# Optimization experiments

Hardware: AMD Instinct MI355X
Metric: run time of the kernel (lower is better)

Reference implementation:

```python
import jax, jax.numpy as jnp
import numpy as np

OUT_DIM = 512

def setup_inputs() -> dict:
    key = jax.random.key(0)
    ks = jax.random.split(key, 8)
    B, C1, C2, H, W, D = 8, 768, 768, 48, 48, OUT_DIM
    x = jax.random.normal(ks[0], (B, C1, H, W), dtype=jnp.float32)
    xt = jax.random.normal(ks[1], (B, C2, H, W), dtype=jnp.float32)
    # nn.Linear params: weight [out, in], bias [out]
    def lin(k, fan_in, fan_out):
        bound = 1.0 / np.sqrt(fan_in)
        kw, kb = jax.random.split(k)
        w = jax.random.uniform(kw, (fan_out, fan_in), jnp.float32, -bound, bound)
        b = jax.random.uniform(kb, (fan_out,), jnp.float32, -bound, bound)
        return w, b
    wq, bq = lin(ks[2], C1, D)
    wk, bk = lin(ks[3], C2, D)
    wv, bv = lin(ks[4], C2, D)
    return {"x": x, "xt": xt, "wq": wq, "bq": bq, "wk": wk, "bk": bk, "wv": wv, "bv": bv}

def reference(x, xt, wq, bq, wk, bk, wv, bv):
    B, C1, H, W = x.shape
    D = wq.shape[0]
    # flatten(2).transpose(1,2): [B, C, H, W] -> [B, H*W, C]
    xs = x.reshape(B, C1, H * W).transpose(0, 2, 1)
    xts = xt.reshape(B, xt.shape[1], -1).transpose(0, 2, 1)
    Q = jnp.einsum('bsc,dc->bsd', xs, wq) + bq   # [B, S, D]
    K = jnp.einsum('btc,dc->btd', xts, wk) + bk  # [B, T, D]
    V = jnp.einsum('btc,dc->btd', xts, wv) + bv  # [B, T, D]
    scores = jnp.einsum('bsd,btd->bst', Q, K) / jnp.sqrt(jnp.float32(D))
    attn = jax.nn.softmax(scores, axis=-1)  # dropout omitted (eval mode)
    return jnp.einsum('bst,btd->bsd', attn, V)
```

## Files before the change

kernel.cpp:

```cpp
#include <hip/hip_runtime.h>
#include <stdint.h>


typedef __bf16 bf16x8 __attribute__((ext_vector_type(8)));
typedef float f32x4 __attribute__((ext_vector_type(4)));

__device__ __forceinline__ unsigned short f2bf(float f) {
  union { float f; unsigned int u; } c; c.f = f;
  return (unsigned short)((c.u + 0x7fffu + ((c.u >> 16) & 1u)) >> 16);
}

#define GLOAD(gp, lp)                                                          \
  __builtin_amdgcn_global_load_lds(                                            \
      (const __attribute__((address_space(1))) void*)(gp),                     \
      (__attribute__((address_space(3))) void*)(lp), 16, 0, 0)

__global__ __launch_bounds__(256) void convw3_kernel(const float* __restrict__ wq,
                                                     const float* __restrict__ wk,
                                                     const float* __restrict__ wv,
                                                     unsigned short* __restrict__ wcat) {
  int i = (blockIdx.x * 256 + threadIdx.x) * 4;
  const float* src = (i < 393216) ? wq : (i < 786432) ? wk : wv;
  const int off = (i < 393216) ? 0 : (i < 786432) ? 393216 : 786432;
  const float4 v = *reinterpret_cast<const float4*>(src + (i - off));
  wcat[i + 0] = f2bf(v.x); wcat[i + 1] = f2bf(v.y);
  wcat[i + 2] = f2bf(v.z); wcat[i + 3] = f2bf(v.w);
}

__global__ __launch_bounds__(256) void init_kernel(const float* __restrict__ bq,
                                                   const float* __restrict__ bk,
                                                   const float* __restrict__ bv,
                                                   float* __restrict__ denom,
                                                   float* __restrict__ bcat) {
  int i = blockIdx.x * 256 + threadIdx.x;
  if (i < 18432) denom[i] = 0.0f;
  else if (i < 19968) {
    int k = i - 18432;
    bcat[k] = (k < 512) ? bq[k] : (k < 1024) ? bk[k - 512] : bv[k - 1024];
  }
}

__global__ __launch_bounds__(256) void transpose_bf16_kernel(
    const float* __restrict__ x, const float* __restrict__ xt,
    unsigned short* __restrict__ xs, unsigned short* __restrict__ xts) {
  const int S = 2304, C = 768;
  const int z = blockIdx.z;
  const float* src = (z < 8) ? x : xt;
  unsigned short* dst = (z < 8) ? xs : xts;
  const int b = z & 7;
  src += (size_t)b * C * S;
  dst += (size_t)b * S * C;
  __shared__ float tile[64][65];
  const int s0 = blockIdx.x * 64, c0 = blockIdx.y * 64;
  const int ls = threadIdx.x & 63, lr = threadIdx.x >> 6;
#pragma unroll
  for (int i = 0; i < 16; ++i) {
    const int c = lr + i * 4;
    tile[c][ls] = src[(size_t)(c0 + c) * S + s0 + ls];
  }
  __syncthreads();
#pragma unroll
  for (int i = 0; i < 16; ++i) {
    const int s = lr + i * 4;
    dst[(size_t)(s0 + s) * C + c0 + ls] = f2bf(tile[ls][s]);
  }
}


__device__ __forceinline__ void stage_half8(
    unsigned short* __restrict__ lds, const unsigned short* __restrict__ gb,
    int ldg, int tK, int side, int h, int tid, int swcol) {
  const int d = tK & 1;
  unsigned short* l0 = lds + (size_t)((d * 4 + side * 2 + h) * 8192);
  const unsigned short* g =
      gb + (size_t)(h * 128 + (tid >> 3)) * ldg + tK * 64 + swcol;
  GLOAD(g, l0 + (size_t)tid * 8);
  GLOAD(g + (size_t)64 * ldg, l0 + (size_t)(tid + 512) * 8);
}

#define RD(baseB, rh, cb)                                        \
  (*reinterpret_cast<const bf16x8*>(                             \
      reinterpret_cast<const char*>(lds) + (baseB) + (rh)*128 + (cb)))

#define PH_READ_A0(ABASE)                              \
  _Pragma("unroll") for (int mf = 0; mf < 4; ++mf) {   \
    a[mf][0] = RD(ABASE, mf * 16 + fr, cb0);           \
    a[mf][1] = RD(ABASE, mf * 16 + fr, cb1);           \
  }
#define PH_READ_A4(ABASE)                              \
  _Pragma("unroll") for (int mf = 0; mf < 4; ++mf) {   \
    a[mf][0] = RD(ABASE, 64 + mf * 16 + fr, cb0);      \
    a[mf][1] = RD(ABASE, 64 + mf * 16 + fr, cb1);      \
  }
#define PH_READ_B01(BBASE)                             \
  _Pragma("unroll") for (int nf = 0; nf < 2; ++nf) {   \
    b01[nf][0] = RD(BBASE, brh + nf * 16, cb0);        \
    b01[nf][1] = RD(BBASE, brh + nf * 16, cb1);        \
  }
#define PH_READ_B23(BBASE)                             \
  _Pragma("unroll") for (int nf = 0; nf < 2; ++nf) {   \
    b23[nf][0] = RD(BBASE, brh + 32 + nf * 16, cb0);   \
    b23[nf][1] = RD(BBASE, brh + 32 + nf * 16, cb1);   \
  }

#define BARRIER_MFMA(MB, NB, BF)                                      \
  __builtin_amdgcn_s_barrier();                                       \
  asm volatile("s_waitcnt lgkmcnt(0)" ::: "memory");                  \
  __builtin_amdgcn_sched_barrier(0);                                  \
  __builtin_amdgcn_s_setprio(1);                                      \
  _Pragma("unroll") for (int mf = 0; mf < 4; ++mf) {                  \
    acc[MB + mf][NB + 0] = __builtin_amdgcn_mfma_f32_16x16x32_bf16(   \
        a[mf][0], BF[0][0], acc[MB + mf][NB + 0], 0, 0, 0);           \
    acc[MB + mf][NB + 0] = __builtin_amdgcn_mfma_f32_16x16x32_bf16(   \
        a[mf][1], BF[0][1], acc[MB + mf][NB + 0], 0, 0, 0);           \
    acc[MB + mf][NB + 1] = __builtin_amdgcn_mfma_f32_16x16x32_bf16(   \
        a[mf][0], BF[1][0], acc[MB + mf][NB + 1], 0, 0, 0);           \
    acc[MB + mf][NB + 1] = __builtin_amdgcn_mfma_f32_16x16x32_bf16(   \
        a[mf][1], BF[1][1], acc[MB + mf][NB + 1], 0, 0, 0);           \
  }                                                                   \
  __builtin_amdgcn_s_setprio(0);                                      \
  __builtin_amdgcn_s_barrier();

template <int NT>
__device__ __forceinline__ void gemm8_core(
    const unsigned short* __restrict__ Ab, const unsigned short* __restrict__ Bb,
    int lda, int ldb, unsigned short* __restrict__ lds, f32x4 (&acc)[8][4]) {
  const int t = threadIdx.x;
  const int lane = t & 63, wid = t >> 6;
  const int wr = wid >> 2, wc = wid & 3;
  const int fr = lane & 15, fq = lane >> 4;
  const int swm = (fr & 7) << 4;
  const int cb0 = (fq * 16) ^ swm;
  const int cb1 = (64 + fq * 16) ^ swm;
  const int brh = (wc & 1) * 64 + fr;
  const int aB0 = (0 + wr) * 16384, aB1 = (4 + wr) * 16384;
  const int bB0 = (2 + (wc >> 1)) * 16384, bB1 = (6 + (wc >> 1)) * 16384;
  const int swcol = (((t & 7) ^ ((t >> 3) & 7))) * 8;

  bf16x8 a[4][2], b01[2][2], b23[2][2];

  stage_half8(lds, Bb, ldb, 0, 1, 0, t, swcol);
  stage_half8(lds, Bb, ldb, 0, 1, 1, t, swcol);
  stage_half8(lds, Ab, lda, 0, 0, 0, t, swcol);
  stage_half8(lds, Ab, lda, 0, 0, 1, t, swcol);
  stage_half8(lds, Bb, ldb, 1, 1, 0, t, swcol);
  stage_half8(lds, Bb, ldb, 1, 1, 1, t, swcol);
  asm volatile("s_waitcnt vmcnt(4)" ::: "memory");
  __builtin_amdgcn_s_barrier();

  const int NI = NT / 2;
#pragma unroll 1
  for (int i = 0; i < NI; ++i) {
    const bool more = (i + 1 < NI);
    const int tu1 = 2 * i + 1, tu2 = 2 * i + 2, tu3 = 2 * i + 3;
    PH_READ_B01(bB0); PH_READ_A0(aB0);
    stage_half8(lds, Ab, lda, tu1, 0, 0, t, swcol);
    BARRIER_MFMA(0, 0, b01);
    PH_READ_B23(bB0);
    stage_half8(lds, Ab, lda, tu1, 0, 1, t, swcol);
    BARRIER_MFMA(0, 2, b23);
    PH_READ_A4(aB0);
    if (more) stage_half8(lds, Bb, ldb, tu2, 1, 0, t, swcol);
    BARRIER_MFMA(4, 2, b23);
    if (more) {
      stage_half8(lds, Bb, ldb, tu2, 1, 1, t, swcol);
      asm volatile("s_waitcnt vmcnt(4)" ::: "memory");
    } else {
      asm volatile("s_waitcnt vmcnt(0)" ::: "memory");
    }
    BARRIER_MFMA(4, 0, b01);
    PH_READ_B01(bB1); PH_READ_A0(aB1);
    if (more) stage_half8(lds, Ab, lda, tu2, 0, 0, t, swcol);
    BARRIER_MFMA(0, 0, b01);
    PH_READ_B23(bB1);
    if (more) stage_half8(lds, Ab, lda, tu2, 0, 1, t, swcol);
    BARRIER_MFMA(0, 2, b23);
    PH_READ_A4(aB1);
    if (more) stage_half8(lds, Bb, ldb, tu3, 1, 0, t, swcol);
    BARRIER_MFMA(4, 2, b23);
    if (more) {
      stage_half8(lds, Bb, ldb, tu3, 1, 1, t, swcol);
      asm volatile("s_waitcnt vmcnt(4)" ::: "memory");
    }
    BARRIER_MFMA(4, 0, b01);
  }
}

__global__ __launch_bounds__(512) void qkv8_kernel(
    const unsigned short* __restrict__ xs, const unsigned short* __restrict__ xts,
    const unsigned short* __restrict__ wcat, const float* __restrict__ bcat,
    unsigned short* __restrict__ Q, unsigned short* __restrict__ K,
    unsigned short* __restrict__ Vt) {
  extern __shared__ unsigned short lds[];
  const int lin = blockIdx.x + 6 * (blockIdx.y + 9 * blockIdx.z);
  const int b = lin & 7, idx = lin >> 3;
  const int byp = idx / 6, bxp = idx - byp * 6;
  const int m0 = byp * 256, n0 = bxp * 256;
  const int seg = n0 >> 9;
  const unsigned short* Ab =
      ((seg == 0) ? xs : xts) + (size_t)b * 2304 * 768 + (size_t)m0 * 768;
  const unsigned short* Bb = wcat + (size_t)n0 * 768;
  f32x4 acc[8][4] = {};
  gemm8_core<12>(Ab, Bb, 768, 768, lds, acc);

  const int t = threadIdx.x;
  const int lane = t & 63, wid = t >> 6;
  const int wr = wid >> 2, wc = wid & 3;
  const int fr = lane & 15, fq = lane >> 4;
  if (seg < 2) {
    unsigned short* Cp = ((seg == 0) ? Q : K) + (size_t)b * 2304 * 512;
#pragma unroll
    for (int nf = 0; nf < 4; ++nf) {
      const int ng = n0 + wc * 64 + nf * 16 + fr;
      const float bj = bcat[ng];
      const int col = ng - seg * 512;
#pragma unroll
      for (int mf = 0; mf < 8; ++mf) {
        const int rbase = m0 + wr * 128 + mf * 16 + fq * 4;
#pragma unroll
        for (int r = 0; r < 4; ++r)
          Cp[(size_t)(rbase + r) * 512 + col] = f2bf(acc[mf][nf][r] + bj);
      }
    }
  } else {
    unsigned short* Cp = Vt + (size_t)b * 512 * 2304;
#pragma unroll
    for (int nf = 0; nf < 4; ++nf) {
      const int ng = n0 + wc * 64 + nf * 16 + fr;
      const float bj = bcat[ng];
      const int d = ng - 1024;
#pragma unroll
      for (int mf = 0; mf < 8; ++mf) {
        const int tb = m0 + wr * 128 + mf * 16 + fq * 4;
        ushort4 pk;
        pk.x = f2bf(acc[mf][nf][0] + bj);
        pk.y = f2bf(acc[mf][nf][1] + bj);
        pk.z = f2bf(acc[mf][nf][2] + bj);
        pk.w = f2bf(acc[mf][nf][3] + bj);
        *reinterpret_cast<ushort4*>(&Cp[(size_t)d * 2304 + tb]) = pk;
      }
    }
  }
}

__global__ __launch_bounds__(512) void scores8_kernel(
    const unsigned short* __restrict__ Qm, const unsigned short* __restrict__ Km,
    float* __restrict__ denom, unsigned short* __restrict__ P) {
  extern __shared__ unsigned short lds[];
  const int lin = blockIdx.x + 9 * (blockIdx.y + 9 * blockIdx.z);
  const int b = lin & 7, idx = lin >> 3;
  const int bxp = idx / 9, byp = idx - bxp * 9;
  const int m0 = byp * 256, n0 = bxp * 256;
  const unsigned short* Ab = Qm + (size_t)b * 2304 * 512 + (size_t)m0 * 512;
  const unsigned short* Bb = Km + (size_t)b * 2304 * 512 + (size_t)n0 * 512;
  f32x4 acc[8][4] = {};
  gemm8_core<8>(Ab, Bb, 512, 512, lds, acc);

  const int t = threadIdx.x;
  const int lane = t & 63, wid = t >> 6;
  const int wr = wid >> 2, wc = wid & 3;
  const int fr = lane & 15, fq = lane >> 4;
  unsigned short* Pp = P + (size_t)b * 2304 * 2304;
  const float SC = 0.044194173824159216f;
#pragma unroll
  for (int mf = 0; mf < 8; ++mf) {
    float rs[4] = {0.f, 0.f, 0.f, 0.f};
    const int rbase = m0 + wr * 128 + mf * 16 + fq * 4;
#pragma unroll
    for (int nf = 0; nf < 4; ++nf) {
      const int col = n0 + wc * 64 + nf * 16 + fr;
#pragma unroll
      for (int r = 0; r < 4; ++r) {
        const float e = __expf(acc[mf][nf][r] * SC - 4.0f);
        rs[r] += e;
        Pp[(size_t)(rbase + r) * 2304 + col] = f2bf(e);
      }
    }
#pragma unroll
    for (int r = 0; r < 4; ++r) {
      float s = rs[r];
#pragma unroll
      for (int o = 8; o >= 1; o >>= 1) s += __shfl_xor(s, o, 16);
      if (fr == 0) atomicAdd(&denom[(size_t)b * 2304 + rbase + r], s);
    }
  }
}

__global__ __launch_bounds__(512) void pv8_kernel(
    const unsigned short* __restrict__ P, const unsigned short* __restrict__ Vt,
    const float* __restrict__ denom, float* __restrict__ Out) {
  extern __shared__ unsigned short lds[];
  const int lin = blockIdx.x + 2 * (blockIdx.y + 9 * blockIdx.z);
  const int b = lin & 7, idx = lin >> 3;
  const int byp = idx >> 1, bxp = idx & 1;
  const int m0 = byp * 256, n0 = bxp * 256;
  const unsigned short* Ab = P + (size_t)b * 2304 * 2304 + (size_t)m0 * 2304;
  const unsigned short* Bb = Vt + (size_t)b * 512 * 2304 + (size_t)n0 * 2304;
  f32x4 acc[8][4] = {};
  gemm8_core<36>(Ab, Bb, 2304, 2304, lds, acc);

  const int t = threadIdx.x;
  const int lane = t & 63, wid = t >> 6;
  const int wr = wid >> 2, wc = wid & 3;
  const int fr = lane & 15, fq = lane >> 4;
  float* Cp = Out + (size_t)b * 2304 * 512;
  const float* dn = denom + (size_t)b * 2304;
#pragma unroll
  for (int mf = 0; mf < 8; ++mf) {
    const int rbase = m0 + wr * 128 + mf * 16 + fq * 4;
#pragma unroll
    for (int r = 0; r < 4; ++r) {
      const float inv = 1.0f / dn[rbase + r];
#pragma unroll
      for (int nf = 0; nf < 4; ++nf) {
        const int col = n0 + wc * 64 + nf * 16 + fr;
        Cp[(size_t)(rbase + r) * 512 + col] = acc[mf][nf][r] * inv;
      }
    }
  }
}

extern "C" void kernel_launch(void* const* d_in, const int* in_sizes, int n_in,
                              void* d_out, int out_size, void* d_ws, size_t ws_size,
                              hipStream_t stream) {
  const float* x  = (const float*)d_in[0];
  const float* xt = (const float*)d_in[1];
  const float* wq = (const float*)d_in[2];
  const float* bq = (const float*)d_in[3];
  const float* wk = (const float*)d_in[4];
  const float* bk = (const float*)d_in[5];
  const float* wv = (const float*)d_in[6];
  const float* bv = (const float*)d_in[7];
  float* out = (float*)d_out;
  unsigned short* ws = (unsigned short*)d_ws;

  unsigned short* Q    = ws;
  unsigned short* Kb   = ws + 9437184;
  unsigned short* Vt   = ws + 18874368;
  unsigned short* P    = ws + 28311552;
  unsigned short* xs   = ws + 28311552;
  unsigned short* xts  = ws + 42467328;
  unsigned short* wcat = ws + 56623104;
  float* bcat  = (float*)(ws + 57802752);
  float* denom = (float*)(ws + 70778880);

  static int attr_set = 0;
  if (!attr_set) {
    hipFuncSetAttribute((const void*)qkv8_kernel,
                        hipFuncAttributeMaxDynamicSharedMemorySize, 131072);
    hipFuncSetAttribute((const void*)scores8_kernel,
                        hipFuncAttributeMaxDynamicSharedMemorySize, 131072);
    hipFuncSetAttribute((const void*)pv8_kernel,
                        hipFuncAttributeMaxDynamicSharedMemorySize, 131072);
    attr_set = 1;
  }

  convw3_kernel<<<1152, 256, 0, stream>>>(wq, wk, wv, wcat);
  init_kernel<<<78, 256, 0, stream>>>(bq, bk, bv, denom, bcat);
  transpose_bf16_kernel<<<dim3(36, 12, 16), 256, 0, stream>>>(x, xt, xs, xts);

  qkv8_kernel<<<dim3(6, 9, 8), 512, 131072, stream>>>(xs, xts, wcat, bcat, Q, Kb, Vt);

  scores8_kernel<<<dim3(9, 9, 8), 512, 131072, stream>>>(Q, Kb, denom, P);

  pv8_kernel<<<dim3(2, 9, 8), 512, 131072, stream>>>(P, Vt, denom, out);
}
```

Baseline: 218.9 us.

## Make scores kernel loop over three column tiles per block sharing pipeline

Each scores block now computes three consecutive 256-wide column tiles of K for the same Q row tile, running one continuous 24-step pipelined K loop. It writes the exp tile and denominator atomics after every 8 k-steps, then zeroes the accumulators. The grid drops from 648 to 216 blocks, which cuts per-block prologue and pipeline fill-drain costs and reuses the Q tile's L2 locality. The cost is fewer blocks per CU on a 256-CU part, so occupancy and tail balance may suffer, and the epilogue stores now stall the pipeline mid-loop.

```diff
diff --git a/kernel.cpp b/kernel.cpp
--- a/kernel.cpp
+++ b/kernel.cpp
@@ -69,11 +69,11 @@
 
 __device__ __forceinline__ void stage_half8(
     unsigned short* __restrict__ lds, const unsigned short* __restrict__ gb,
-    int ldg, int tK, int side, int h, int tid, int swcol) {
+    int ldg, int tK, size_t koff, int side, int h, int tid, int swcol) {
   const int d = tK & 1;
   unsigned short* l0 = lds + (size_t)((d * 4 + side * 2 + h) * 8192);
   const unsigned short* g =
-      gb + (size_t)(h * 128 + (tid >> 3)) * ldg + tK * 64 + swcol;
+      gb + (size_t)(h * 128 + (tid >> 3)) * ldg + koff + swcol;
   GLOAD(g, l0 + (size_t)tid * 8);
   GLOAD(g + (size_t)64 * ldg, l0 + (size_t)(tid + 512) * 8);
 }
@@ -121,30 +121,32 @@
   __builtin_amdgcn_s_setprio(0);                                      \
   __builtin_amdgcn_s_barrier();
 
+#define CORE_CTX()                                                    \
+  const int t = threadIdx.x;                                          \
+  const int lane = t & 63, wid = t >> 6;                              \
+  const int wr = wid >> 2, wc = wid & 3;                              \
+  const int fr = lane & 15, fq = lane >> 4;                           \
+  const int swm = (fr & 7) << 4;                                      \
+  const int cb0 = (fq * 16) ^ swm;                                    \
+  const int cb1 = (64 + fq * 16) ^ swm;                               \
+  const int brh = (wc & 1) * 64 + fr;                                 \
+  const int aB0 = (0 + wr) * 16384, aB1 = (4 + wr) * 16384;           \
+  const int bB0 = (2 + (wc >> 1)) * 16384, bB1 = (6 + (wc >> 1)) * 16384; \
+  const int swcol = (((t & 7) ^ ((t >> 3) & 7))) * 8;
+
 template <int NT>
 __device__ __forceinline__ void gemm8_core(
     const unsigned short* __restrict__ Ab, const unsigned short* __restrict__ Bb,
     int lda, int ldb, unsigned short* __restrict__ lds, f32x4 (&acc)[8][4]) {
-  const int t = threadIdx.x;
-  const int lane = t & 63, wid = t >> 6;
-  const int wr = wid >> 2, wc = wid & 3;
-  const int fr = lane & 15, fq = lane >> 4;
-  const int swm = (fr & 7) << 4;
-  const int cb0 = (fq * 16) ^ swm;
-  const int cb1 = (64 + fq * 16) ^ swm;
-  const int brh = (wc & 1) * 64 + fr;
-  const int aB0 = (0 + wr) * 16384, aB1 = (4 + wr) * 16384;
-  const int bB0 = (2 + (wc >> 1)) * 16384, bB1 = (6 + (wc >> 1)) * 16384;
-  const int swcol = (((t & 7) ^ ((t >> 3) & 7))) * 8;
-
+  CORE_CTX();
   bf16x8 a[4][2], b01[2][2], b23[2][2];
 
-  stage_half8(lds, Bb, ldb, 0, 1, 0, t, swcol);
-  stage_half8(lds, Bb, ldb, 0, 1, 1, t, swcol);
-  stage_half8(lds, Ab, lda, 0, 0, 0, t, swcol);
-  stage_half8(lds, Ab, lda, 0, 0, 1, t, swcol);
-  stage_half8(lds, Bb, ldb, 1, 1, 0, t, swcol);
-  stage_half8(lds, Bb, ldb, 1, 1, 1, t, swcol);
+  stage_half8(lds, Bb, ldb, 0, 0, 1, 0, t, swcol);
+  stage_half8(lds, Bb, ldb, 0, 0, 1, 1, t, swcol);
+  stage_half8(lds, Ab, lda, 0, 0, 0, 0, t, swcol);
+  stage_half8(lds, Ab, lda, 0, 0, 0, 1, t, swcol);
+  stage_half8(lds, Bb, ldb, 1, 64, 1, 0, t, swcol);
+  stage_half8(lds, Bb, ldb, 1, 64, 1, 1, t, swcol);
   asm volatile("s_waitcnt vmcnt(4)" ::: "memory");
   __builtin_amdgcn_s_barrier();
 
@@ -154,32 +156,32 @@
     const bool more = (i + 1 < NI);
     const int tu1 = 2 * i + 1, tu2 = 2 * i + 2, tu3 = 2 * i + 3;
     PH_READ_B01(bB0); PH_READ_A0(aB0);
-    stage_half8(lds, Ab, lda, tu1, 0, 0, t, swcol);
+    stage_half8(lds, Ab, lda, tu1, (size_t)tu1 * 64, 0, 0, t, swcol);
     BARRIER_MFMA(0, 0, b01);
     PH_READ_B23(bB0);
-    stage_half8(lds, Ab, lda, tu1, 0, 1, t, swcol);
+    stage_half8(lds, Ab, lda, tu1, (size_t)tu1 * 64, 0, 1, t, swcol);
     BARRIER_MFMA(0, 2, b23);
     PH_READ_A4(aB0);
-    if (more) stage_half8(lds, Bb, ldb, tu2, 1, 0, t, swcol);
+    if (more) stage_half8(lds, Bb, ldb, tu2, (size_t)tu2 * 64, 1, 0, t, swcol);
     BARRIER_MFMA(4, 2, b23);
     if (more) {
-      stage_half8(lds, Bb, ldb, tu2, 1, 1, t, swcol);
+      stage_half8(lds, Bb, ldb, tu2, (size_t)tu2 * 64, 1, 1, t, swcol);
       asm volatile("s_waitcnt vmcnt(4)" ::: "memory");
     } else {
       asm volatile("s_waitcnt vmcnt(0)" ::: "memory");
     }
     BARRIER_MFMA(4, 0, b01);
     PH_READ_B01(bB1); PH_READ_A0(aB1);
-    if (more) stage_half8(lds, Ab, lda, tu2, 0, 0, t, swcol);
+    if (more) stage_half8(lds, Ab, lda, tu2, (size_t)tu2 * 64, 0, 0, t, swcol);
     BARRIER_MFMA(0, 0, b01);
     PH_READ_B23(bB1);
-    if (more) stage_half8(lds, Ab, lda, tu2, 0, 1, t, swcol);
+    if (more) stage_half8(lds, Ab, lda, tu2, (size_t)tu2 * 64, 0, 1, t, swcol);
     BARRIER_MFMA(0, 2, b23);
     PH_READ_A4(aB1);
-    if (more) stage_half8(lds, Bb, ldb, tu3, 1, 0, t, swcol);
+    if (more) stage_half8(lds, Bb, ldb, tu3, (size_t)tu3 * 64, 1, 0, t, swcol);
     BARRIER_MFMA(4, 2, b23);
     if (more) {
-      stage_half8(lds, Bb, ldb, tu3, 1, 1, t, swcol);
+      stage_half8(lds, Bb, ldb, tu3, (size_t)tu3 * 64, 1, 1, t, swcol);
       asm volatile("s_waitcnt vmcnt(4)" ::: "memory");
     }
     BARRIER_MFMA(4, 0, b01);
@@ -243,45 +245,100 @@
   }
 }
 
+#define AKOFF(tt) ((size_t)((tt) & 7) * 64)
+#define BKOFF(tt) ((size_t)((tt) >> 3) * 131072 + (size_t)((tt) & 7) * 64)
 __global__ __launch_bounds__(512) void scores8_kernel(
     const unsigned short* __restrict__ Qm, const unsigned short* __restrict__ Km,
     float* __restrict__ denom, unsigned short* __restrict__ P) {
   extern __shared__ unsigned short lds[];
-  const int lin = blockIdx.x + 9 * (blockIdx.y + 9 * blockIdx.z);
+  const int lin = blockIdx.x + 3 * (blockIdx.y + 9 * blockIdx.z);
   const int b = lin & 7, idx = lin >> 3;
   const int bxp = idx / 9, byp = idx - bxp * 9;
-  const int m0 = byp * 256, n0 = bxp * 256;
+  const int m0 = byp * 256, nb = bxp * 768;
   const unsigned short* Ab = Qm + (size_t)b * 2304 * 512 + (size_t)m0 * 512;
-  const unsigned short* Bb = Km + (size_t)b * 2304 * 512 + (size_t)n0 * 512;
+  const unsigned short* Bb = Km + (size_t)b * 2304 * 512 + (size_t)nb * 512;
   f32x4 acc[8][4] = {};
-  gemm8_core<8>(Ab, Bb, 512, 512, lds, acc);
-
-  const int t = threadIdx.x;
-  const int lane = t & 63, wid = t >> 6;
-  const int wr = wid >> 2, wc = wid & 3;
-  const int fr = lane & 15, fq = lane >> 4;
+  CORE_CTX();
+  bf16x8 a[4][2], b01[2][2], b23[2][2];
+
   unsigned short* Pp = P + (size_t)b * 2304 * 2304;
+  float* dn = denom + (size_t)b * 2304;
   const float SC = 0.044194173824159216f;
-#pragma unroll
-  for (int mf = 0; mf < 8; ++mf) {
-    float rs[4] = {0.f, 0.f, 0.f, 0.f};
-    const int rbase = m0 + wr * 128 + mf * 16 + fq * 4;
-#pragma unroll
-    for (int nf = 0; nf < 4; ++nf) {
-      const int col = n0 + wc * 64 + nf * 16 + fr;
-#pragma unroll
-      for (int r = 0; r < 4; ++r) {
-        const float e = __expf(acc[mf][nf][r] * SC - 4.0f);
-        rs[r] += e;
-        Pp[(size_t)(rbase + r) * 2304 + col] = f2bf(e);
+
+  stage_half8(lds, Bb, 512, 0, BKOFF(0), 1, 0, t, swcol);
+  stage_half8(lds, Bb, 512, 0, BKOFF(0), 1, 1, t, swcol);
+  stage_half8(lds, Ab, 512, 0, AKOFF(0), 0, 0, t, swcol);
+  stage_half8(lds, Ab, 512, 0, AKOFF(0), 0, 1, t, swcol);
+  stage_half8(lds, Bb, 512, 1, BKOFF(1), 1, 0, t, swcol);
+  stage_half8(lds, Bb, 512, 1, BKOFF(1), 1, 1, t, swcol);
+  asm volatile("s_waitcnt vmcnt(4)" ::: "memory");
+  __builtin_amdgcn_s_barrier();
+
+#pragma unroll 1
+  for (int i = 0; i < 12; ++i) {
+    const bool more = (i + 1 < 12);
+    const int tu1 = 2 * i + 1, tu2 = 2 * i + 2, tu3 = 2 * i + 3;
+    PH_READ_B01(bB0); PH_READ_A0(aB0);
+    stage_half8(lds, Ab, 512, tu1, AKOFF(tu1), 0, 0, t, swcol);
+    BARRIER_MFMA(0, 0, b01);
+    PH_READ_B23(bB0);
+    stage_half8(lds, Ab, 512, tu1, AKOFF(tu1), 0, 1, t, swcol);
+    BARRIER_MFMA(0, 2, b23);
+    PH_READ_A4(aB0);
+    if (more) stage_half8(lds, Bb, 512, tu2, BKOFF(tu2), 1, 0, t, swcol);
+    BARRIER_MFMA(4, 2, b23);
+    if (more) {
+      stage_half8(lds, Bb, 512, tu2, BKOFF(tu2), 1, 1, t, swcol);
+      asm volatile("s_waitcnt vmcnt(4)" ::: "memory");
+    } else {
+      asm volatile("s_waitcnt vmcnt(0)" ::: "memory");
+    }
+    BARRIER_MFMA(4, 0, b01);
+    PH_READ_B01(bB1); PH_READ_A0(aB1);
+    if (more) stage_half8(lds, Ab, 512, tu2, AKOFF(tu2), 0, 0, t, swcol);
+    BARRIER_MFMA(0, 0, b01);
+    PH_READ_B23(bB1);
+    if (more) stage_half8(lds, Ab, 512, tu2, AKOFF(tu2), 0, 1, t, swcol);
+    BARRIER_MFMA(0, 2, b23);
+    PH_READ_A4(aB1);
+    if (more) stage_half8(lds, Bb, 512, tu3, BKOFF(tu3), 1, 0, t, swcol);
+    BARRIER_MFMA(4, 2, b23);
+    if (more) {
+      stage_half8(lds, Bb, 512, tu3, BKOFF(tu3), 1, 1, t, swcol);
+      asm volatile("s_waitcnt vmcnt(4)" ::: "memory");
+    }
+    BARRIER_MFMA(4, 0, b01);
+
+    if ((i & 3) == 3) {
+      const int cbase = nb + (i >> 2) * 256;
+#pragma unroll
+      for (int mf = 0; mf < 8; ++mf) {
+        float rs[4] = {0.f, 0.f, 0.f, 0.f};
+        const int rbase = m0 + wr * 128 + mf * 16 + fq * 4;
+#pragma unroll
+        for (int nf = 0; nf < 4; ++nf) {
+          const int col = cbase + wc * 64 + nf * 16 + fr;
+#pragma unroll
+          for (int r = 0; r < 4; ++r) {
+            const float e = __expf(acc[mf][nf][r] * SC - 4.0f);
+            rs[r] += e;
+            Pp[(size_t)(rbase + r) * 2304 + col] = f2bf(e);
+          }
+        }
+#pragma unroll
+        for (int r = 0; r < 4; ++r) {
+          float s = rs[r];
+#pragma unroll
+          for (int o = 8; o >= 1; o >>= 1) s += __shfl_xor(s, o, 16);
+          if (fr == 0) atomicAdd(&dn[rbase + r], s);
+        }
       }
-    }
-#pragma unroll
-    for (int r = 0; r < 4; ++r) {
-      float s = rs[r];
-#pragma unroll
-      for (int o = 8; o >= 1; o >>= 1) s += __shfl_xor(s, o, 16);
-      if (fr == 0) atomicAdd(&denom[(size_t)b * 2304 + rbase + r], s);
+#pragma unroll
+      for (int mf = 0; mf < 8; ++mf)
+#pragma unroll
+        for (int nf = 0; nf < 4; ++nf)
+#pragma unroll
+          for (int r = 0; r < 4; ++r) acc[mf][nf][r] = 0.0f;
     }
   }
 }
@@ -361,7 +418,7 @@
 
   qkv8_kernel<<<dim3(6, 9, 8), 512, 131072, stream>>>(xs, xts, wcat, bcat, Q, Kb, Vt);
 
-  scores8_kernel<<<dim3(9, 9, 8), 512, 131072, stream>>>(Q, Kb, denom, P);
+  scores8_kernel<<<dim3(3, 9, 8), 512, 131072, stream>>>(Q, Kb, denom, P);
 
   pv8_kernel<<<dim3(2, 9, 8), 512, 131072, stream>>>(P, Vt, denom, out);
 }
```

New measurement: 233.7 us. +6.8%, slower.

## Compute softmax denominators via ones-MFMA inside PV GEMM instead of atomics

Applied to the files above, without the earlier changes.

Removes the per-row exp-sum reduction and atomicAdd into a global denominator buffer from the scores kernel, and drops the denom zeroing from the init kernel. The PV kernel instead accumulates row sums of the bf16 P tile by issuing extra MFMAs against a vector of ones, so the denominator comes from the same rounded P values used in the numerator. This trades shuffles, atomics and a global buffer for about 12.5% more MFMA work in the PV GEMM.

```diff
diff --git a/kernel.cpp b/kernel.cpp
--- a/kernel.cpp
+++ b/kernel.cpp
@@ -30,14 +30,10 @@
 __global__ __launch_bounds__(256) void init_kernel(const float* __restrict__ bq,
                                                    const float* __restrict__ bk,
                                                    const float* __restrict__ bv,
-                                                   float* __restrict__ denom,
                                                    float* __restrict__ bcat) {
-  int i = blockIdx.x * 256 + threadIdx.x;
-  if (i < 18432) denom[i] = 0.0f;
-  else if (i < 19968) {
-    int k = i - 18432;
+  int k = blockIdx.x * 256 + threadIdx.x;
+  if (k < 1536)
     bcat[k] = (k < 512) ? bq[k] : (k < 1024) ? bk[k - 512] : bv[k - 1024];
-  }
 }
 
 __global__ __launch_bounds__(256) void transpose_bf16_kernel(
@@ -103,7 +99,7 @@
     b23[nf][1] = RD(BBASE, brh + 32 + nf * 16, cb1);   \
   }
 
-#define BARRIER_MFMA(MB, NB, BF)                                      \
+#define BARRIER_MFMA(MB, NB, BF, DS)                                  \
   __builtin_amdgcn_s_barrier();                                       \
   asm volatile("s_waitcnt lgkmcnt(0)" ::: "memory");                  \
   __builtin_amdgcn_sched_barrier(0);                                  \
@@ -118,13 +114,24 @@
     acc[MB + mf][NB + 1] = __builtin_amdgcn_mfma_f32_16x16x32_bf16(   \
         a[mf][1], BF[1][1], acc[MB + mf][NB + 1], 0, 0, 0);           \
   }                                                                   \
+  if constexpr (DSUM) {                                               \
+    if constexpr (DS) {                                               \
+      _Pragma("unroll") for (int mf = 0; mf < 4; ++mf) {              \
+        accd[MB + mf] = __builtin_amdgcn_mfma_f32_16x16x32_bf16(      \
+            a[mf][0], vones, accd[MB + mf], 0, 0, 0);                 \
+        accd[MB + mf] = __builtin_amdgcn_mfma_f32_16x16x32_bf16(      \
+            a[mf][1], vones, accd[MB + mf], 0, 0, 0);                 \
+      }                                                               \
+    }                                                                 \
+  }                                                                   \
   __builtin_amdgcn_s_setprio(0);                                      \
   __builtin_amdgcn_s_barrier();
 
-template <int NT>
+template <int NT, bool DSUM>
 __device__ __forceinline__ void gemm8_core(
     const unsigned short* __restrict__ Ab, const unsigned short* __restrict__ Bb,
-    int lda, int ldb, unsigned short* __restrict__ lds, f32x4 (&acc)[8][4]) {
+    int lda, int ldb, unsigned short* __restrict__ lds, f32x4 (&acc)[8][4],
+    f32x4 (&accd)[8]) {
   const int t = threadIdx.x;
   const int lane = t & 63, wid = t >> 6;
   const int wr = wid >> 2, wc = wid & 3;
@@ -138,6 +145,13 @@
   const int swcol = (((t & 7) ^ ((t >> 3) & 7))) * 8;
 
   bf16x8 a[4][2], b01[2][2], b23[2][2];
+  bf16x8 vones;
+  {
+    unsigned short os = 0x3F80;
+#pragma unroll
+    for (int j = 0; j < 8; ++j)
+      reinterpret_cast<unsigned short*>(&vones)[j] = os;
+  }
 
   stage_half8(lds, Bb, ldb, 0, 1, 0, t, swcol);
   stage_half8(lds, Bb, ldb, 0, 1, 1, t, swcol);
@@ -155,34 +169,34 @@
     const int tu1 = 2 * i + 1, tu2 = 2 * i + 2, tu3 = 2 * i + 3;
     PH_READ_B01(bB0); PH_READ_A0(aB0);
     stage_half8(lds, Ab, lda, tu1, 0, 0, t, swcol);
-    BARRIER_MFMA(0, 0, b01);
+    BARRIER_MFMA(0, 0, b01, 1);
     PH_READ_B23(bB0);
     stage_half8(lds, Ab, lda, tu1, 0, 1, t, swcol);
-    BARRIER_MFMA(0, 2, b23);
+    BARRIER_MFMA(0, 2, b23, 0);
     PH_READ_A4(aB0);
     if (more) stage_half8(lds, Bb, ldb, tu2, 1, 0, t, swcol);
-    BARRIER_MFMA(4, 2, b23);
+    BARRIER_MFMA(4, 2, b23, 1);
     if (more) {
       stage_half8(lds, Bb, ldb, tu2, 1, 1, t, swcol);
       asm volatile("s_waitcnt vmcnt(4)" ::: "memory");
     } else {
       asm volatile("s_waitcnt vmcnt(0)" ::: "memory");
     }
-    BARRIER_MFMA(4, 0, b01);
+    BARRIER_MFMA(4, 0, b01, 0);
     PH_READ_B01(bB1); PH_READ_A0(aB1);
     if (more) stage_half8(lds, Ab, lda, tu2, 0, 0, t, swcol);
-    BARRIER_MFMA(0, 0, b01);
+    BARRIER_MFMA(0, 0, b01, 1);
     PH_READ_B23(bB1);
     if (more) stage_half8(lds, Ab, lda, tu2, 0, 1, t, swcol);
-    BARRIER_MFMA(0, 2, b23);
+    BARRIER_MFMA(0, 2, b23, 0);
     PH_READ_A4(aB1);
     if (more) stage_half8(lds, Bb, ldb, tu3, 1, 0, t, swcol);
-    BARRIER_MFMA(4, 2, b23);
+    BARRIER_MFMA(4, 2, b23, 1);
     if (more) {
       stage_half8(lds, Bb, ldb, tu3, 1, 1, t, swcol);
       asm volatile("s_waitcnt vmcnt(4)" ::: "memory");
     }
-    BARRIER_MFMA(4, 0, b01);
+    BARRIER_MFMA(4, 0, b01, 0);
   }
 }
 
@@ -201,7 +215,8 @@
       ((seg == 0) ? xs : xts) + (size_t)b * 2304 * 768 + (size_t)m0 * 768;
   const unsigned short* Bb = wcat + (size_t)n0 * 768;
   f32x4 acc[8][4] = {};
-  gemm8_core<12>(Ab, Bb, 768, 768, lds, acc);
+  f32x4 accd[8] = {};
+  gemm8_core<12, false>(Ab, Bb, 768, 768, lds, acc, accd);
 
   const int t = threadIdx.x;
   const int lane = t & 63, wid = t >> 6;
@@ -245,7 +260,7 @@
 
 __global__ __launch_bounds__(512) void scores8_kernel(
     const unsigned short* __restrict__ Qm, const unsigned short* __restrict__ Km,
-    float* __restrict__ denom, unsigned short* __restrict__ P) {
+    unsigned short* __restrict__ P) {
   extern __shared__ unsigned short lds[];
   const int lin = blockIdx.x + 9 * (blockIdx.y + 9 * blockIdx.z);
   const int b = lin & 7, idx = lin >> 3;
@@ -254,7 +269,8 @@
   const unsigned short* Ab = Qm + (size_t)b * 2304 * 512 + (size_t)m0 * 512;
   const unsigned short* Bb = Km + (size_t)b * 2304 * 512 + (size_t)n0 * 512;
   f32x4 acc[8][4] = {};
-  gemm8_core<8>(Ab, Bb, 512, 512, lds, acc);
+  f32x4 accd[8] = {};
+  gemm8_core<8, false>(Ab, Bb, 512, 512, lds, acc, accd);
 
   const int t = threadIdx.x;
   const int lane = t & 63, wid = t >> 6;
@@ -264,31 +280,21 @@
   const float SC = 0.044194173824159216f;
 #pragma unroll
   for (int mf = 0; mf < 8; ++mf) {
-    float rs[4] = {0.f, 0.f, 0.f, 0.f};
     const int rbase = m0 + wr * 128 + mf * 16 + fq * 4;
 #pragma unroll
     for (int nf = 0; nf < 4; ++nf) {
       const int col = n0 + wc * 64 + nf * 16 + fr;
 #pragma unroll
-      for (int r = 0; r < 4; ++r) {
-        const float e = __expf(acc[mf][nf][r] * SC - 4.0f);
-        rs[r] += e;
-        Pp[(size_t)(rbase + r) * 2304 + col] = f2bf(e);
-      }
-    }
-#pragma unroll
-    for (int r = 0; r < 4; ++r) {
-      float s = rs[r];
-#pragma unroll
-      for (int o = 8; o >= 1; o >>= 1) s += __shfl_xor(s, o, 16);
-      if (fr == 0) atomicAdd(&denom[(size_t)b * 2304 + rbase + r], s);
+      for (int r = 0; r < 4; ++r)
+        Pp[(size_t)(rbase + r) * 2304 + col] =
+            f2bf(__expf(acc[mf][nf][r] * SC - 4.0f));
     }
   }
 }
 
 __global__ __launch_bounds__(512) void pv8_kernel(
     const unsigned short* __restrict__ P, const unsigned short* __restrict__ Vt,
-    const float* __restrict__ denom, float* __restrict__ Out) {
+    float* __restrict__ Out) {
   extern __shared__ unsigned short lds[];
   const int lin = blockIdx.x + 2 * (blockIdx.y + 9 * blockIdx.z);
   const int b = lin & 7, idx = lin >> 3;
@@ -297,20 +303,20 @@
   const unsigned short* Ab = P + (size_t)b * 2304 * 2304 + (size_t)m0 * 2304;
   const unsigned short* Bb = Vt + (size_t)b * 512 * 2304 + (size_t)n0 * 2304;
   f32x4 acc[8][4] = {};
-  gemm8_core<36>(Ab, Bb, 2304, 2304, lds, acc);
+  f32x4 accd[8] = {};
+  gemm8_core<36, true>(Ab, Bb, 2304, 2304, lds, acc, accd);
 
   const int t = threadIdx.x;
   const int lane = t & 63, wid = t >> 6;
   const int wr = wid >> 2, wc = wid & 3;
   const int fr = lane & 15, fq = lane >> 4;
   float* Cp = Out + (size_t)b * 2304 * 512;
-  const float* dn = denom + (size_t)b * 2304;
 #pragma unroll
   for (int mf = 0; mf < 8; ++mf) {
     const int rbase = m0 + wr * 128 + mf * 16 + fq * 4;
 #pragma unroll
     for (int r = 0; r < 4; ++r) {
-      const float inv = 1.0f / dn[rbase + r];
+      const float inv = 1.0f / accd[mf][r];
 #pragma unroll
       for (int nf = 0; nf < 4; ++nf) {
         const int col = n0 + wc * 64 + nf * 16 + fr;
@@ -342,7 +348,6 @@
   unsigned short* xts  = ws + 42467328;
   unsigned short* wcat = ws + 56623104;
   float* bcat  = (float*)(ws + 57802752);
-  float* denom = (float*)(ws + 70778880);
 
   static int attr_set = 0;
   if (!attr_set) {
@@ -356,12 +361,12 @@
   }
 
   convw3_kernel<<<1152, 256, 0, stream>>>(wq, wk, wv, wcat);
-  init_kernel<<<78, 256, 0, stream>>>(bq, bk, bv, denom, bcat);
+  init_kernel<<<6, 256, 0, stream>>>(bq, bk, bv, bcat);
   transpose_bf16_kernel<<<dim3(36, 12, 16), 256, 0, stream>>>(x, xt, xs, xts);
 
   qkv8_kernel<<<dim3(6, 9, 8), 512, 131072, stream>>>(xs, xts, wcat, bcat, Q, Kb, Vt);
 
-  scores8_kernel<<<dim3(9, 9, 8), 512, 131072, stream>>>(Q, Kb, denom, P);
-
-  pv8_kernel<<<dim3(2, 9, 8), 512, 131072, stream>>>(P, Vt, denom, out);
-}
+  scores8_kernel<<<dim3(9, 9, 8), 512, 131072, stream>>>(Q, Kb, P);
+
+  pv8_kernel<<<dim3(2, 9, 8), 512, 131072, stream>>>(P, Vt, out);
+}
```

Result: slower. 256.1 us (+17.0%).
